# Kernel optimization log

Measured on AMD Instinct MI355X. Metric: run time of the kernel, lower is better.

The kernel has to match this reference:

```python
import jax, jax.numpy as jnp
import numpy as np

HEADS = 16
DIM_HEAD = 64
DIM = 1024
INNER = HEADS * DIM_HEAD  # 1024


def setup_inputs() -> dict:
    key = jax.random.key(0)
    ks = jax.random.split(key, 8)
    B, N, M = 4, 2048, 2048
    x = jax.random.normal(ks[0], (B, N, DIM), dtype=jnp.float32)
    context = jax.random.normal(ks[1], (B, M, DIM), dtype=jnp.float32)
    x_mask = (jax.random.uniform(ks[2], (B, N)) > 0.1).astype(jnp.float32)
    context_mask = (jax.random.uniform(ks[3], (B, M)) > 0.1).astype(jnp.float32)
    s = 0.02
    Wq = jax.random.normal(ks[4], (DIM, INNER), dtype=jnp.float32) * s
    Wkv = jax.random.normal(ks[5], (DIM, 2 * INNER), dtype=jnp.float32) * s
    Wo = jax.random.normal(ks[6], (INNER, DIM), dtype=jnp.float32) * s
    bo = jnp.zeros((DIM,), dtype=jnp.float32)
    return {"x": x, "context": context, "x_mask": x_mask,
            "context_mask": context_mask, "Wq": Wq, "Wkv": Wkv, "Wo": Wo, "bo": bo}


def _split_heads(t):
    b, n, _ = t.shape
    return t.reshape(b, n, HEADS, DIM_HEAD).transpose(0, 2, 1, 3)  # b h n d


def reference(x, context, x_mask, context_mask, Wq, Wkv, Wo, bo):
    scale = DIM_HEAD ** -0.5
    q = _split_heads(x @ Wq)                       # b h n d
    kv = context @ Wkv
    k = _split_heads(kv[..., :INNER])              # b h m d
    v = _split_heads(kv[..., INNER:])              # b h m d
    dots = jnp.einsum('bhnd,bhmd->bhnm', q, k) * scale
    # attn_bias = 1 - x_mask ⊗ context_mask; masked where isclose(attn_bias, 1)
    prod = x_mask[:, None, :, None] * context_mask[:, None, None, :]  # b 1 n m
    masked = jnp.isclose(1.0 - prod, 1.0)          # b 1 n m, broadcast over heads
    dots = jnp.where(masked, -jnp.inf, dots)       # b h n m
    # rows with no valid key: zero the whole row before softmax
    valid = jnp.any(~masked, axis=-1, keepdims=True)  # b 1 n 1
    dots = jnp.where(valid, dots, 0.0)
    attn = jax.nn.softmax(dots, axis=-1)
    attn = jnp.where(valid, attn, 0.0)
    out = jnp.einsum('bhnm,bhmd->bhnd', attn, v)
    b, h, n, d = out.shape
    out = out.transpose(0, 2, 1, 3).reshape(b, n, h * d)
    return out @ Wo + bo
```

## Files before the change

### kernel.cpp

```cpp
#include <hip/hip_runtime.h>

#define DEVI __device__ __forceinline__

typedef __attribute__((ext_vector_type(4))) float f32x4;
typedef __attribute__((ext_vector_type(8))) short s16x8;
typedef __attribute__((ext_vector_type(8))) _Float16 f16x8;
typedef __attribute__((ext_vector_type(2))) _Float16 f16x2;

#if __has_builtin(__builtin_amdgcn_exp2f)
#define EXP2F __builtin_amdgcn_exp2f
#else
#define EXP2F exp2f
#endif

DEVI ushort f2h(float f) {
  _Float16 h = (_Float16)f;
  return __builtin_bit_cast(ushort, h);
}

DEVI unsigned pkrtz(float a, float b) {
  return __builtin_bit_cast(unsigned, __builtin_amdgcn_cvt_pkrtz(a, b));
}

DEVI float dot2acc(unsigned pk, float acc) {
#if __has_builtin(__builtin_amdgcn_fdot2)
  f16x2 one2 = {(_Float16)1.0f, (_Float16)1.0f};
  return __builtin_amdgcn_fdot2(__builtin_bit_cast(f16x2, pk), one2, acc, false);
#else
  f16x2 v = __builtin_bit_cast(f16x2, pk);
  return acc + (float)v[0] + (float)v[1];
#endif
}

DEVI void gload_lds16(const void* g, void* l) {
  typedef const unsigned int GlobU __attribute__((address_space(1)));
  typedef unsigned int LdsU __attribute__((address_space(3)));
  __builtin_amdgcn_global_load_lds((GlobU*)g, (LdsU*)l, 16, 0, 0);
}

__global__ __launch_bounds__(256) void cast_f16_kernel(
    const float4* __restrict__ x, const float4* __restrict__ ctx,
    ushort4* __restrict__ xo, ushort4* __restrict__ co) {
  int i = blockIdx.x * 256 + threadIdx.x;
  const float4* src;
  ushort4* dst;
  int j;
  if (i < 2097152) { src = x; dst = xo; j = i; }
  else             { src = ctx; dst = co; j = i - 2097152; }
  float4 v = src[j];
  ushort4 o;
  o.x = f2h(v.x); o.y = f2h(v.y); o.z = f2h(v.z); o.w = f2h(v.w);
  dst[j] = o;
}

__global__ __launch_bounds__(256) void transpose_cast_kernel(
    const float* __restrict__ Wq, const float* __restrict__ Wkv,
    const float* __restrict__ Wo, ushort* __restrict__ WqT,
    ushort* __restrict__ WkvT, ushort* __restrict__ WoT) {
  __shared__ ushort tile[64][65];
  int bx = blockIdx.x;
  const float* in; ushort* out; int C, cb;
  if (bx < 16)      { in = Wq;  out = WqT;  C = 1024; cb = bx * 64; }
  else if (bx < 48) { in = Wkv; out = WkvT; C = 2048; cb = (bx - 16) * 64; }
  else              { in = Wo;  out = WoT;  C = 1024; cb = (bx - 48) * 64; }
  const int R = 1024;
  int rb = blockIdx.y * 64;
  int t = threadIdx.x;
  int c4 = (t & 15) * 4, r0 = t >> 4;
#pragma unroll
  for (int i = 0; i < 4; i++) {
    int r = r0 + i * 16;
    float4 v = *(const float4*)(in + (size_t)(rb + r) * C + cb + c4);
    tile[r][c4 + 0] = f2h(v.x);
    tile[r][c4 + 1] = f2h(v.y);
    tile[r][c4 + 2] = f2h(v.z);
    tile[r][c4 + 3] = f2h(v.w);
  }
  __syncthreads();
#pragma unroll
  for (int i = 0; i < 4; i++) {
    int rr = r0 + i * 16;
    ushort4 o;
    o.x = tile[c4 + 0][rr]; o.y = tile[c4 + 1][rr];
    o.z = tile[c4 + 2][rr]; o.w = tile[c4 + 3][rr];
    *(ushort4*)(out + (size_t)(cb + rr) * R + rb + c4) = o;
  }
}

DEVI void gemm_core(const ushort* __restrict__ A, const ushort* __restrict__ Bt,
                    int K, int rowbase, int colbase, int tid,
                    ushort* As, ushort* Bs, f32x4 acc[4][4]) {
  const int lane = tid & 63, wave = tid >> 6;
  const int quad = lane >> 4, ln = lane & 15;
  const int wrow = (wave >> 1) * 64, wcol = (wave & 1) * 64;
  for (int k0 = 0; k0 < K; k0 += 32) {
    __syncthreads();
#pragma unroll
    for (int i = 0; i < 2; i++) {
      int f = i * 256 + tid;
      int r = f >> 2;
      int c = (f & 3) ^ (r & 3);
      gload_lds16(A + (size_t)(rowbase + r) * K + (k0 + c * 8),
                  (char*)As + (size_t)(i * 256 + wave * 64) * 16);
      gload_lds16(Bt + (size_t)(colbase + r) * K + (k0 + c * 8),
                  (char*)Bs + (size_t)(i * 256 + wave * 64) * 16);
    }
    __syncthreads();
    f16x8 a[4], b[4];
#pragma unroll
    for (int mt = 0; mt < 4; mt++) {
      int r = wrow + mt * 16 + ln;
      a[mt] = *(const f16x8*)(As + ((size_t)r * 4 + (quad ^ (r & 3))) * 8);
    }
#pragma unroll
    for (int nt = 0; nt < 4; nt++) {
      int r = wcol + nt * 16 + ln;
      b[nt] = *(const f16x8*)(Bs + ((size_t)r * 4 + (quad ^ (r & 3))) * 8);
    }
#pragma unroll
    for (int mt = 0; mt < 4; mt++)
#pragma unroll
      for (int nt = 0; nt < 4; nt++)
        acc[mt][nt] = __builtin_amdgcn_mfma_f32_16x16x32_f16(a[mt], b[nt], acc[mt][nt], 0, 0, 0);
  }
}

__global__ __launch_bounds__(256, 2) void qkv_gemm(
    const ushort* __restrict__ xb, const ushort* __restrict__ cb,
    const ushort* __restrict__ WqT, const ushort* __restrict__ WkvT,
    ushort* __restrict__ Qo, ushort* __restrict__ Ko, ushort* __restrict__ Vo) {
  __shared__ ushort As[128 * 32];
  __shared__ ushort Bs[128 * 32];
  const int tid = threadIdx.x;
  const int lane = tid & 63, wave = tid >> 6;
  const int quad = lane >> 4, ln = lane & 15;
  const int bx = blockIdx.x;
  const bool isQ = bx < 8;
  const int colbase = (isQ ? bx : bx - 8) * 128;
  const int rowbase = blockIdx.y * 128;
  const int wrow = (wave >> 1) * 64, wcol = (wave & 1) * 64;
  f32x4 acc[4][4] = {};
  gemm_core(isQ ? xb : cb, isQ ? WqT : WkvT, 1024, rowbase, colbase, tid, As, Bs, acc);

  if (isQ) {
    const float qscale = 0.18033688011112042f;
#pragma unroll
    for (int nt = 0; nt < 4; nt++) {
      int col = colbase + wcol + nt * 16 + ln;
      int h = col >> 6, d = col & 63;
#pragma unroll
      for (int mt = 0; mt < 4; mt++) {
        int row = rowbase + wrow + mt * 16 + quad * 4;
#pragma unroll
        for (int r = 0; r < 4; r++) {
          int rr = row + r;
          int bb = rr >> 11, n = rr & 2047;
          Qo[(((size_t)bb * 16 + h) * 2048 + n) * 64 + d] = f2h(acc[mt][nt][r] * qscale);
        }
      }
    }
  } else {
    bool isK = (colbase < 1024);
#pragma unroll
    for (int nt = 0; nt < 4; nt++) {
      int col = colbase + wcol + nt * 16 + ln;
#pragma unroll
      for (int mt = 0; mt < 4; mt++) {
        int row = rowbase + wrow + mt * 16 + quad * 4;
        int bb = row >> 11, m = row & 2047;
        if (isK) {
          int h = col >> 6, d = col & 63;
#pragma unroll
          for (int r = 0; r < 4; r++)
            Ko[(((size_t)bb * 16 + h) * 2048 + (m + r)) * 64 + d] = f2h(acc[mt][nt][r]);
        } else {
          int c2 = col - 1024;
          int h = c2 >> 6, d = c2 & 63;
          uint2 pv;
          pv.x = pkrtz(acc[mt][nt][0], acc[mt][nt][1]);
          pv.y = pkrtz(acc[mt][nt][2], acc[mt][nt][3]);
          *(uint2*)(Vo + (((size_t)bb * 16 + h) * 64 + d) * 2048 + m) = pv;
        }
      }
    }
  }
}

__global__ __launch_bounds__(256, 2) void out_gemm(
    const ushort* __restrict__ A, const ushort* __restrict__ Bt,
    float* __restrict__ C, const float* __restrict__ bias) {
  __shared__ ushort As[128 * 32];
  __shared__ ushort Bs[128 * 32];
  const int tid = threadIdx.x;
  const int lane = tid & 63, wave = tid >> 6;
  const int quad = lane >> 4, ln = lane & 15;
  const int colbase = blockIdx.x * 128, rowbase = blockIdx.y * 128;
  const int wrow = (wave >> 1) * 64, wcol = (wave & 1) * 64;
  f32x4 acc[4][4] = {};
  gemm_core(A, Bt, 1024, rowbase, colbase, tid, As, Bs, acc);
#pragma unroll
  for (int nt = 0; nt < 4; nt++) {
    int col = colbase + wcol + nt * 16 + ln;
    float bv = bias[col];
#pragma unroll
    for (int mt = 0; mt < 4; mt++) {
      int row = rowbase + wrow + mt * 16 + quad * 4;
#pragma unroll
      for (int r = 0; r < 4; r++)
        C[(size_t)(row + r) * 1024 + col] = acc[mt][nt][r] + bv;
    }
  }
}

__global__ __launch_bounds__(256, 2) void attn_kernel(
    const ushort* __restrict__ Q, const ushort* __restrict__ K,
    const ushort* __restrict__ VT, const float* __restrict__ xmask,
    const float* __restrict__ cmask, ushort* __restrict__ O) {
  __shared__ ushort Ks[64 * 64];
  __shared__ ushort Vs[64 * 64];
  __shared__ ushort Ps[4 * 64 * 72];
  const int tid = threadIdx.x, lane = tid & 63, wave = tid >> 6;
  const int quad = lane >> 4, ln = lane & 15;
  const int bid = blockIdx.x;
  const int qb = bid & 7, h = (bid >> 3) & 15, b = bid >> 7;
  const size_t bh = (size_t)b * 16 + h;
  const ushort* Qbh = Q + bh * (2048 * 64);
  const ushort* Kbh = K + bh * (2048 * 64);
  const ushort* Vbh = VT + bh * (64 * 2048);
  const int q0 = qb * 256 + wave * 64;

  f16x8 qf[4][2];
#pragma unroll
  for (int qt = 0; qt < 4; qt++)
#pragma unroll
    for (int kc = 0; kc < 2; kc++)
      qf[qt][kc] = *(const f16x8*)(Qbh + (size_t)(q0 + qt * 16 + ln) * 64 + kc * 32 + quad * 8);

  float xm[4];
#pragma unroll
  for (int qt = 0; qt < 4; qt++) xm[qt] = xmask[b * 2048 + q0 + qt * 16 + ln];

  f32x4 o[4][4] = {};
  float lrun[4] = {0.f, 0.f, 0.f, 0.f};

  for (int kb = 0; kb < 32; kb++) {
    const int m0 = kb * 64;
    __syncthreads();
#pragma unroll
    for (int i = 0; i < 2; i++) {
      int f = i * 256 + tid;
      int r = f >> 3;
      int c = (f & 7) ^ (r & 7);
      gload_lds16(Kbh + (size_t)(m0 + r) * 64 + c * 8,
                  (char*)Ks + (size_t)(i * 256 + wave * 64) * 16);
      gload_lds16(Vbh + (size_t)r * 2048 + (m0 + c * 8),
                  (char*)Vs + (size_t)(i * 256 + wave * 64) * 16);
    }
    f32x4 bias4[4];
#pragma unroll
    for (int kt = 0; kt < 4; kt++) {
      float4 cm = *(const float4*)(cmask + b * 2048 + m0 + kt * 16 + quad * 4);
      bias4[kt][0] = fmaf(cm.x, 3.0e4f, -3.0e4f);
      bias4[kt][1] = fmaf(cm.y, 3.0e4f, -3.0e4f);
      bias4[kt][2] = fmaf(cm.z, 3.0e4f, -3.0e4f);
      bias4[kt][3] = fmaf(cm.w, 3.0e4f, -3.0e4f);
    }
    __syncthreads();

    f32x4 s[4][4];
#pragma unroll
    for (int kt = 0; kt < 4; kt++)
#pragma unroll
      for (int qt = 0; qt < 4; qt++) s[kt][qt] = bias4[kt];
#pragma unroll
    for (int kc = 0; kc < 2; kc++) {
#pragma unroll
      for (int kt = 0; kt < 4; kt++) {
        int r = kt * 16 + ln;
        f16x8 ka = *(const f16x8*)(Ks + ((size_t)r * 8 + ((kc * 4 + quad) ^ (r & 7))) * 8);
#pragma unroll
        for (int qt = 0; qt < 4; qt++)
          s[kt][qt] = __builtin_amdgcn_mfma_f32_16x16x32_f16(ka, qf[qt][kc], s[kt][qt], 0, 0, 0);
      }
    }

#pragma unroll
    for (int qt = 0; qt < 4; qt++) {
      int qrow = qt * 16 + ln;
      ushort* pb = Ps + wave * (64 * 72) + qrow * 72;
      float rs = 0.f;
#pragma unroll
      for (int kt = 0; kt < 4; kt++) {
        float p0 = EXP2F(s[kt][qt][0]);
        float p1 = EXP2F(s[kt][qt][1]);
        float p2 = EXP2F(s[kt][qt][2]);
        float p3 = EXP2F(s[kt][qt][3]);
        uint2 pv;
        pv.x = pkrtz(p0, p1);
        pv.y = pkrtz(p2, p3);
        rs = dot2acc(pv.x, rs);
        rs = dot2acc(pv.y, rs);
        *(uint2*)(pb + (kt * 4 + quad) * 4) = pv;
      }
      rs += __shfl_xor(rs, 16, 64);
      rs += __shfl_xor(rs, 32, 64);
      lrun[qt] += rs;
    }
    __builtin_amdgcn_s_waitcnt(0);

#pragma unroll
    for (int kc = 0; kc < 2; kc++) {
      f16x8 pf[4];
#pragma unroll
      for (int qt = 0; qt < 4; qt++) {
        int qrow = qt * 16 + ln;
        pf[qt] = *(const f16x8*)(Ps + wave * (64 * 72) + qrow * 72 + (kc * 8 + quad * 2) * 4);
      }
#pragma unroll
      for (int dt = 0; dt < 4; dt++) {
        int r = dt * 16 + ln;
        f16x8 va = *(const f16x8*)(Vs + ((size_t)r * 8 + ((kc * 4 + quad) ^ (r & 7))) * 8);
#pragma unroll
        for (int qt = 0; qt < 4; qt++)
          o[dt][qt] = __builtin_amdgcn_mfma_f32_16x16x32_f16(va, pf[qt], o[dt][qt], 0, 0, 0);
      }
    }
  }

#pragma unroll
  for (int qt = 0; qt < 4; qt++) {
    float inv = (xm[qt] != 0.f && lrun[qt] > 0.f) ? (1.f / lrun[qt]) : 0.f;
    int n = q0 + qt * 16 + ln;
    ushort* ob = O + ((size_t)(b * 2048 + n) * 16 + h) * 64;
#pragma unroll
    for (int dt = 0; dt < 4; dt++) {
      uint2 pv;
      pv.x = pkrtz(o[dt][qt][0] * inv, o[dt][qt][1] * inv);
      pv.y = pkrtz(o[dt][qt][2] * inv, o[dt][qt][3] * inv);
      *(uint2*)(ob + dt * 16 + quad * 4) = pv;
    }
  }
}

extern "C" void kernel_launch(void* const* d_in, const int* in_sizes, int n_in,
                              void* d_out, int out_size, void* d_ws, size_t ws_size,
                              hipStream_t stream) {
  const float* x   = (const float*)d_in[0];
  const float* ctx = (const float*)d_in[1];
  const float* xm  = (const float*)d_in[2];
  const float* cm  = (const float*)d_in[3];
  const float* Wq  = (const float*)d_in[4];
  const float* Wkv = (const float*)d_in[5];
  const float* Wo  = (const float*)d_in[6];
  const float* bo  = (const float*)d_in[7];

  char* ws = (char*)d_ws;
  const size_t MB = 1024 * 1024;
  ushort* xb   = (ushort*)(ws + 0);
  ushort* cb   = (ushort*)(ws + 16 * MB);
  ushort* WqT  = (ushort*)(ws + 32 * MB);
  ushort* WkvT = (ushort*)(ws + 34 * MB);
  ushort* WoT  = (ushort*)(ws + 38 * MB);
  ushort* Qb   = (ushort*)(ws + 40 * MB);
  ushort* Kb   = (ushort*)(ws + 56 * MB);
  ushort* VTb  = (ushort*)(ws + 72 * MB);
  ushort* Ob   = xb;

  cast_f16_kernel<<<16384, 256, 0, stream>>>((const float4*)x, (const float4*)ctx,
                                             (ushort4*)xb, (ushort4*)cb);
  transpose_cast_kernel<<<dim3(64, 16), 256, 0, stream>>>(Wq, Wkv, Wo, WqT, WkvT, WoT);
  qkv_gemm<<<dim3(24, 64), 256, 0, stream>>>(xb, cb, WqT, WkvT, Qb, Kb, VTb);
  attn_kernel<<<512, 256, 0, stream>>>(Qb, Kb, VTb, xm, cm, Ob);
  out_gemm<<<dim3(8, 64), 256, 0, stream>>>(Ob, WoT, (float*)d_out, bo);
}
```

Measured before the change: 340.1 us.

## Double-buffer K/V tiles in LDS and precompute context-mask bias

```diff
diff --git a/kernel.cpp b/kernel.cpp
--- a/kernel.cpp
+++ b/kernel.cpp
@@ -3,7 +3,6 @@
 #define DEVI __device__ __forceinline__
 
 typedef __attribute__((ext_vector_type(4))) float f32x4;
-typedef __attribute__((ext_vector_type(8))) short s16x8;
 typedef __attribute__((ext_vector_type(8))) _Float16 f16x8;
 typedef __attribute__((ext_vector_type(2))) _Float16 f16x2;
 
@@ -216,9 +215,10 @@
     const ushort* __restrict__ Q, const ushort* __restrict__ K,
     const ushort* __restrict__ VT, const float* __restrict__ xmask,
     const float* __restrict__ cmask, ushort* __restrict__ O) {
-  __shared__ ushort Ks[64 * 64];
-  __shared__ ushort Vs[64 * 64];
-  __shared__ ushort Ps[4 * 64 * 72];
+  __shared__ ushort Ks[2][64 * 64];
+  __shared__ ushort Vs[2][64 * 64];
+  __shared__ ushort Ps[4 * 64 * 40];
+  __shared__ float CMB[2048];
   const int tid = threadIdx.x, lane = tid & 63, wave = tid >> 6;
   const int quad = lane >> 4, ln = lane & 15;
   const int bid = blockIdx.x;
@@ -229,6 +229,18 @@
   const ushort* Vbh = VT + bh * (64 * 2048);
   const int q0 = qb * 256 + wave * 64;
 
+  {
+    float4 c0 = *(const float4*)(cmask + b * 2048 + tid * 8);
+    float4 c1 = *(const float4*)(cmask + b * 2048 + tid * 8 + 4);
+    float4 b0, b1;
+    b0.x = fmaf(c0.x, 3.0e4f, -3.0e4f); b0.y = fmaf(c0.y, 3.0e4f, -3.0e4f);
+    b0.z = fmaf(c0.z, 3.0e4f, -3.0e4f); b0.w = fmaf(c0.w, 3.0e4f, -3.0e4f);
+    b1.x = fmaf(c1.x, 3.0e4f, -3.0e4f); b1.y = fmaf(c1.y, 3.0e4f, -3.0e4f);
+    b1.z = fmaf(c1.z, 3.0e4f, -3.0e4f); b1.w = fmaf(c1.w, 3.0e4f, -3.0e4f);
+    *(float4*)(CMB + tid * 8) = b0;
+    *(float4*)(CMB + tid * 8 + 4) = b1;
+  }
+
   f16x8 qf[4][2];
 #pragma unroll
   for (int qt = 0; qt < 4; qt++)
@@ -240,32 +252,39 @@
 #pragma unroll
   for (int qt = 0; qt < 4; qt++) xm[qt] = xmask[b * 2048 + q0 + qt * 16 + ln];
 
-  f32x4 o[4][4] = {};
-  float lrun[4] = {0.f, 0.f, 0.f, 0.f};
-
-  for (int kb = 0; kb < 32; kb++) {
-    const int m0 = kb * 64;
-    __syncthreads();
+  __syncthreads();
+
+#pragma unroll
+  for (int t = 0; t < 2; t++) {
 #pragma unroll
     for (int i = 0; i < 2; i++) {
       int f = i * 256 + tid;
       int r = f >> 3;
       int c = (f & 7) ^ (r & 7);
-      gload_lds16(Kbh + (size_t)(m0 + r) * 64 + c * 8,
-                  (char*)Ks + (size_t)(i * 256 + wave * 64) * 16);
-      gload_lds16(Vbh + (size_t)r * 2048 + (m0 + c * 8),
-                  (char*)Vs + (size_t)(i * 256 + wave * 64) * 16);
-    }
+      gload_lds16(Kbh + (size_t)(t * 64 + r) * 64 + c * 8,
+                  (char*)Ks[t] + (size_t)(i * 256 + wave * 64) * 16);
+      gload_lds16(Vbh + (size_t)r * 2048 + (t * 64 + c * 8),
+                  (char*)Vs[t] + (size_t)(i * 256 + wave * 64) * 16);
+    }
+  }
+
+  f32x4 o[4][4] = {};
+  float lrun[4] = {0.f, 0.f, 0.f, 0.f};
+
+  for (int kb = 0; kb < 32; kb++) {
+    const int cur = kb & 1;
+    const int m0 = kb * 64;
+    const ushort* KsC = Ks[cur];
+    const ushort* VsC = Vs[cur];
+
+    if (kb < 31) asm volatile("s_waitcnt vmcnt(4)" ::: "memory");
+    else         asm volatile("s_waitcnt vmcnt(0)" ::: "memory");
+    asm volatile("s_barrier" ::: "memory");
+
     f32x4 bias4[4];
 #pragma unroll
-    for (int kt = 0; kt < 4; kt++) {
-      float4 cm = *(const float4*)(cmask + b * 2048 + m0 + kt * 16 + quad * 4);
-      bias4[kt][0] = fmaf(cm.x, 3.0e4f, -3.0e4f);
-      bias4[kt][1] = fmaf(cm.y, 3.0e4f, -3.0e4f);
-      bias4[kt][2] = fmaf(cm.z, 3.0e4f, -3.0e4f);
-      bias4[kt][3] = fmaf(cm.w, 3.0e4f, -3.0e4f);
-    }
-    __syncthreads();
+    for (int kt = 0; kt < 4; kt++)
+      bias4[kt] = *(const f32x4*)(CMB + m0 + kt * 16 + quad * 4);
 
     f32x4 s[4][4];
 #pragma unroll
@@ -277,52 +296,70 @@
 #pragma unroll
       for (int kt = 0; kt < 4; kt++) {
         int r = kt * 16 + ln;
-        f16x8 ka = *(const f16x8*)(Ks + ((size_t)r * 8 + ((kc * 4 + quad) ^ (r & 7))) * 8);
+        f16x8 ka = *(const f16x8*)(KsC + ((size_t)r * 8 + ((kc * 4 + quad) ^ (r & 7))) * 8);
 #pragma unroll
         for (int qt = 0; qt < 4; qt++)
           s[kt][qt] = __builtin_amdgcn_mfma_f32_16x16x32_f16(ka, qf[qt][kc], s[kt][qt], 0, 0, 0);
       }
     }
 
-#pragma unroll
-    for (int qt = 0; qt < 4; qt++) {
-      int qrow = qt * 16 + ln;
-      ushort* pb = Ps + wave * (64 * 72) + qrow * 72;
-      float rs = 0.f;
-#pragma unroll
-      for (int kt = 0; kt < 4; kt++) {
-        float p0 = EXP2F(s[kt][qt][0]);
-        float p1 = EXP2F(s[kt][qt][1]);
-        float p2 = EXP2F(s[kt][qt][2]);
-        float p3 = EXP2F(s[kt][qt][3]);
-        uint2 pv;
-        pv.x = pkrtz(p0, p1);
-        pv.y = pkrtz(p2, p3);
-        rs = dot2acc(pv.x, rs);
-        rs = dot2acc(pv.y, rs);
-        *(uint2*)(pb + (kt * 4 + quad) * 4) = pv;
-      }
-      rs += __shfl_xor(rs, 16, 64);
-      rs += __shfl_xor(rs, 32, 64);
-      lrun[qt] += rs;
-    }
-    __builtin_amdgcn_s_waitcnt(0);
-
+    float rs[4] = {0.f, 0.f, 0.f, 0.f};
 #pragma unroll
     for (int kc = 0; kc < 2; kc++) {
-      f16x8 pf[4];
 #pragma unroll
       for (int qt = 0; qt < 4; qt++) {
         int qrow = qt * 16 + ln;
-        pf[qt] = *(const f16x8*)(Ps + wave * (64 * 72) + qrow * 72 + (kc * 8 + quad * 2) * 4);
+        ushort* pb = Ps + wave * (64 * 40) + qrow * 40;
+#pragma unroll
+        for (int t = 0; t < 2; t++) {
+          int kt = kc * 2 + t;
+          float p0 = EXP2F(s[kt][qt][0]);
+          float p1 = EXP2F(s[kt][qt][1]);
+          float p2 = EXP2F(s[kt][qt][2]);
+          float p3 = EXP2F(s[kt][qt][3]);
+          uint2 pv;
+          pv.x = pkrtz(p0, p1);
+          pv.y = pkrtz(p2, p3);
+          rs[qt] = dot2acc(pv.x, rs[qt]);
+          rs[qt] = dot2acc(pv.y, rs[qt]);
+          *(uint2*)(pb + (t * 4 + quad) * 4) = pv;
+        }
+      }
+      f16x8 pf[4];
+#pragma unroll
+      for (int qt = 0; qt < 4; qt++) {
+        int qrow = qt * 16 + ln;
+        pf[qt] = *(const f16x8*)(Ps + wave * (64 * 40) + qrow * 40 + quad * 8);
       }
 #pragma unroll
       for (int dt = 0; dt < 4; dt++) {
         int r = dt * 16 + ln;
-        f16x8 va = *(const f16x8*)(Vs + ((size_t)r * 8 + ((kc * 4 + quad) ^ (r & 7))) * 8);
+        f16x8 va = *(const f16x8*)(VsC + ((size_t)r * 8 + ((kc * 4 + quad) ^ (r & 7))) * 8);
 #pragma unroll
         for (int qt = 0; qt < 4; qt++)
           o[dt][qt] = __builtin_amdgcn_mfma_f32_16x16x32_f16(va, pf[qt], o[dt][qt], 0, 0, 0);
+      }
+    }
+#pragma unroll
+    for (int qt = 0; qt < 4; qt++) {
+      float r2 = rs[qt];
+      r2 += __shfl_xor(r2, 16, 64);
+      r2 += __shfl_xor(r2, 32, 64);
+      lrun[qt] += r2;
+    }
+
+    asm volatile("s_barrier" ::: "memory");
+    if (kb < 30) {
+      const int m2 = m0 + 128;
+#pragma unroll
+      for (int i = 0; i < 2; i++) {
+        int f = i * 256 + tid;
+        int r = f >> 3;
+        int c = (f & 7) ^ (r & 7);
+        gload_lds16(Kbh + (size_t)(m2 + r) * 64 + c * 8,
+                    (char*)Ks[cur] + (size_t)(i * 256 + wave * 64) * 16);
+        gload_lds16(Vbh + (size_t)r * 2048 + (m2 + c * 8),
+                    (char*)Vs[cur] + (size_t)(i * 256 + wave * 64) * 16);
       }
     }
   }
```

After: 320.7 us. -5.7%, faster.
